# Optimization experiments

Measured on AMD Instinct MI355X. Metric: run time of the kernel, lower is better.

Reference implementation:

```python
import jax, jax.numpy as jnp
import numpy as np

N_NODES = 50000
N_EDGES = 1_600_000
FEAT, HIDDEN, NUM_CLASS = 128, 128, 64


def setup_inputs() -> dict:
    key = jax.random.key(0)
    k1, k2, k3, k4, k5 = jax.random.split(key, 5)
    h = jax.random.normal(k1, (N_NODES, FEAT), dtype=jnp.float32)
    edge_index = jax.random.randint(k2, (2, N_EDGES), 0, N_NODES, dtype=jnp.int32)
    # Glorot-ish init for the three GraphConv weights (bias=False)
    W1 = jax.random.normal(k3, (FEAT, HIDDEN), dtype=jnp.float32) * (1.0 / np.sqrt(FEAT))
    W2 = jax.random.normal(k4, (HIDDEN, HIDDEN), dtype=jnp.float32) * (1.0 / np.sqrt(HIDDEN))
    W3 = jax.random.normal(k5, (HIDDEN, NUM_CLASS), dtype=jnp.float32) * (1.0 / np.sqrt(HIDDEN))
    return {"h": h, "edge_index": edge_index, "W1": W1, "W2": W2, "W3": W3}


def _gcn_layer(h, W, src, dst, out_isqrt, in_isqrt, n_nodes):
    # DGL GraphConv, norm='both', bias=False: relu( D_in^{-1/2} A D_out^{-1/2} h W )
    h = h * out_isqrt[:, None]          # scale source features
    h = h @ W                            # dense projection (order-invariant)
    agg = jax.ops.segment_sum(h[src], dst, num_segments=n_nodes)  # SpMM aggregation
    agg = agg * in_isqrt[:, None]
    return jax.nn.relu(agg)


def reference(h, edge_index, W1, W2, W3):
    src, dst = edge_index[0], edge_index[1]
    ones = jnp.ones(src.shape[0], dtype=h.dtype)
    out_deg = jax.ops.segment_sum(ones, src, num_segments=N_NODES)
    in_deg = jax.ops.segment_sum(ones, dst, num_segments=N_NODES)
    out_isqrt = jnp.clip(out_deg, 1.0, None) ** -0.5
    in_isqrt = jnp.clip(in_deg, 1.0, None) ** -0.5
    h = _gcn_layer(h, W1, src, dst, out_isqrt, in_isqrt, N_NODES)
    h = _gcn_layer(h, W2, src, dst, out_isqrt, in_isqrt, N_NODES)
    h = _gcn_layer(h, W3, src, dst, out_isqrt, in_isqrt, N_NODES)
    return h
```

## Files before the change

### kernel.cpp

```cpp
#include <hip/hip_runtime.h>

#define N_NODES 50000
#define N_EDGES 1600000
#define FEAT 128
#define HIDDEN 128
#define NUM_CLASS 64

#define NBUCK 782
#define EPB 2048
#define NBLK 782
#define SCAP 2560
#define AGG_NBN 3125
#define GEMM_BLOCKS 782

#define HISTROW 50048
#define HISTW (HISTROW / 4)
#define HIST_EPB 6250

typedef _Float16 h8 __attribute__((ext_vector_type(8)));
typedef float f32x4 __attribute__((ext_vector_type(4)));

__global__ __launch_bounds__(256) void passA_kernel(const int* __restrict__ ei,
                                                    unsigned* __restrict__ priv,
                                                    int* __restrict__ localoff,
                                                    int* __restrict__ Cmat) {
    __shared__ int cnt[1024];
    __shared__ int base[1024];
    __shared__ int cur[1024];
    __shared__ int tmp[256];
    __shared__ unsigned sorted[EPB];
    const int t = threadIdx.x;
    const int blk = blockIdx.x;
    for (int i = t; i < 1024; i += 256) cnt[i] = 0;
    __syncthreads();

    const int ebase = blk * EPB;
    unsigned packed[8];
    int bk[8];
#pragma unroll
    for (int j = 0; j < 8; ++j) {
        const int e = ebase + t + j * 256;
        if (e < N_EDGES) {
            const unsigned s = (unsigned)ei[e];
            const unsigned d = (unsigned)ei[N_EDGES + e];
            bk[j] = (int)(d >> 6);
            packed[j] = s | ((d & 63u) << 16) | ((d >> 6) << 22);
            atomicAdd(&cnt[bk[j]], 1);
        } else bk[j] = -1;
    }
    __syncthreads();

    const int c0 = cnt[4*t], c1 = cnt[4*t+1], c2 = cnt[4*t+2], c3 = cnt[4*t+3];
    const int s = c0 + c1 + c2 + c3;
    tmp[t] = s;
    __syncthreads();
    for (int off = 1; off < 256; off <<= 1) {
        int v = (t >= off) ? tmp[t - off] : 0;
        __syncthreads();
        tmp[t] += v;
        __syncthreads();
    }
    const int excl = tmp[t] - s;
    base[4*t] = excl;            cur[4*t] = excl;
    base[4*t+1] = excl+c0;       cur[4*t+1] = excl+c0;
    base[4*t+2] = excl+c0+c1;    cur[4*t+2] = excl+c0+c1;
    base[4*t+3] = excl+c0+c1+c2; cur[4*t+3] = excl+c0+c1+c2;
    __syncthreads();

    for (int b = t; b < NBUCK; b += 256) {
        localoff[(size_t)blk * NBUCK + b] = base[b];
        Cmat[(size_t)blk * NBUCK + b] = cnt[b];
    }
#pragma unroll
    for (int j = 0; j < 8; ++j)
        if (bk[j] >= 0) {
            const int pos = atomicAdd(&cur[bk[j]], 1);
            sorted[pos] = packed[j];
        }
    __syncthreads();
    const int total = min(EPB, N_EDGES - ebase);
    for (int i = t; i < total; i += 256) priv[(size_t)blk * EPB + i] = sorted[i];
}

__global__ __launch_bounds__(256) void hist8_kernel(const int* __restrict__ ei,
                                                    unsigned* __restrict__ hist8) {
    __shared__ unsigned hh[HISTW];
    const int t = threadIdx.x;
    for (int i = t; i < HISTW; i += 256) hh[i] = 0;
    __syncthreads();
    const int base = blockIdx.x * HIST_EPB;
    for (int j = t; j < HIST_EPB; j += 256) {
        const unsigned s = (unsigned)ei[base + j];
        atomicAdd(&hh[s >> 2], 1u << ((s & 3u) * 8u));
    }
    __syncthreads();
    unsigned* dst = hist8 + (size_t)blockIdx.x * HISTW;
    for (int i = t; i < HISTW; i += 256) dst[i] = hh[i];
}

__global__ __launch_bounds__(256) void scales8_kernel(const unsigned* __restrict__ hist8,
                                                      float* __restrict__ out_isqrt) {
    const int w = blockIdx.x * 256 + threadIdx.x;
    if (w >= HISTW) return;
    unsigned s0 = 0, s1 = 0, s2 = 0, s3 = 0;
    for (int b = 0; b < 256; ++b) {
        const unsigned u = hist8[(size_t)b * HISTW + w];
        s0 += u & 255u; s1 += (u >> 8) & 255u; s2 += (u >> 16) & 255u; s3 += u >> 24;
    }
    const int n = w * 4;
    if (n < N_NODES)     out_isqrt[n]     = rsqrtf((float)(s0 < 1 ? 1 : s0));
    if (n + 1 < N_NODES) out_isqrt[n + 1] = rsqrtf((float)(s1 < 1 ? 1 : s1));
    if (n + 2 < N_NODES) out_isqrt[n + 2] = rsqrtf((float)(s2 < 1 ? 1 : s2));
    if (n + 3 < N_NODES) out_isqrt[n + 3] = rsqrtf((float)(s3 < 1 ? 1 : s3));
}

__global__ __launch_bounds__(256) void btotal_kernel(const int* __restrict__ Cmat,
                                                     int* __restrict__ total) {
    __shared__ int red[256];
    const int b = blockIdx.x;
    const int t = threadIdx.x;
    int s = 0;
    for (int blk = t; blk < NBLK; blk += 256) s += Cmat[(size_t)blk * NBUCK + b];
    red[t] = s;
    __syncthreads();
    for (int off = 128; off > 0; off >>= 1) {
        if (t < off) red[t] += red[t + off];
        __syncthreads();
    }
    if (t == 0) total[b] = red[0];
}

__global__ __launch_bounds__(256) void bscan2_kernel(const int* __restrict__ total,
                                                     int* __restrict__ csr_base,
                                                     int* __restrict__ row_off) {
    __shared__ int tt[1024];
    __shared__ int tmp[256];
    const int t = threadIdx.x;
    for (int i = t; i < 1024; i += 256) tt[i] = (i < NBUCK) ? total[i] : 0;
    __syncthreads();
    const int c0 = tt[4*t], c1 = tt[4*t+1], c2 = tt[4*t+2], c3 = tt[4*t+3];
    const int s = c0 + c1 + c2 + c3;
    tmp[t] = s;
    __syncthreads();
    for (int off = 1; off < 256; off <<= 1) {
        int v = (t >= off) ? tmp[t - off] : 0;
        __syncthreads();
        tmp[t] += v;
        __syncthreads();
    }
    const int excl = tmp[t] - s;
    if (4*t < NBUCK)   csr_base[4*t]   = excl;
    if (4*t+1 < NBUCK) csr_base[4*t+1] = excl + c0;
    if (4*t+2 < NBUCK) csr_base[4*t+2] = excl + c0 + c1;
    if (4*t+3 < NBUCK) csr_base[4*t+3] = excl + c0 + c1 + c2;
    if (t == 0) { csr_base[NBUCK] = N_EDGES; row_off[N_NODES] = N_EDGES; }
}

__global__ __launch_bounds__(256) void csr2_kernel(const int* __restrict__ localoff,
                                                   const unsigned* __restrict__ priv,
                                                   const int* __restrict__ csr_base,
                                                   unsigned short* __restrict__ csr,
                                                   int* __restrict__ row_off,
                                                   float* __restrict__ in_isqrt) {
    __shared__ unsigned gath[SCAP];
    __shared__ int tmp[256];
    __shared__ int cnt64[64];
    __shared__ int cur64[64];
    const int b = blockIdx.x;
    const int t = threadIdx.x;

    int off_[4], len_[4];
#pragma unroll
    for (int u = 0; u < 4; ++u) {
        const int blk = 4*t + u;
        if (blk < NBLK) {
            const int o = localoff[(size_t)blk * NBUCK + b];
            const int nxt = (b == NBUCK - 1) ? min(EPB, N_EDGES - blk * EPB)
                                             : localoff[(size_t)blk * NBUCK + b + 1];
            off_[u] = o; len_[u] = nxt - o;
        } else { off_[u] = 0; len_[u] = 0; }
    }
    const int s = len_[0] + len_[1] + len_[2] + len_[3];
    tmp[t] = s;
    __syncthreads();
    for (int off = 1; off < 256; off <<= 1) {
        int v = (t >= off) ? tmp[t - off] : 0;
        __syncthreads();
        tmp[t] += v;
        __syncthreads();
    }
    int run = tmp[t] - s;
    const int total = tmp[255];
#pragma unroll
    for (int u = 0; u < 4; ++u) {
        const int blk = 4*t + u;
        const unsigned* srcp = priv + (size_t)blk * EPB + off_[u];
        for (int j = 0; j < len_[u]; ++j)
            if (run + j < SCAP) gath[run + j] = srcp[j];
        run += len_[u];
    }
    if (t < 64) cnt64[t] = 0;
    __syncthreads();

    const int gtot = min(total, SCAP);
    for (int i = t; i < gtot; i += 256) atomicAdd(&cnt64[(gath[i] >> 16) & 63u], 1);
    __syncthreads();

    const int v64 = (t < 64) ? cnt64[t] : 0;
    tmp[t] = v64;
    __syncthreads();
    for (int off = 1; off < 64; off <<= 1) {
        int v = (t >= off) ? tmp[t - off] : 0;
        __syncthreads();
        tmp[t] += v;
        __syncthreads();
    }
    if (t < 64) {
        const int myoff = csr_base[b] + tmp[t] - v64;
        cur64[t] = myoff;
        const int node = b * 64 + t;
        if (node < N_NODES) {
            row_off[node] = myoff;
            in_isqrt[node] = rsqrtf((float)(v64 > 0 ? v64 : 1));
        }
    }
    __syncthreads();

    for (int i = t; i < gtot; i += 256) {
        const unsigned w = gath[i];
        const int pos = atomicAdd(&cur64[(w >> 16) & 63u], 1);
        csr[pos] = (unsigned short)(w & 0xFFFFu);
    }
}

__global__ __launch_bounds__(256) void wconv_kernel(const float* __restrict__ W1,
                                                    const float* __restrict__ W2,
                                                    const float* __restrict__ W3,
                                                    _Float16* __restrict__ WhT) {
    const int id = blockIdx.x * 256 + threadIdx.x;
    if (id < 16384) {
        const int n = id >> 7, k = id & 127;
        WhT[id] = (_Float16)W1[k * 128 + n];
    } else if (id < 32768) {
        const int i = id - 16384, n = i >> 7, k = i & 127;
        WhT[id] = (_Float16)W2[k * 128 + n];
    } else if (id < 40960) {
        const int i = id - 32768, n = i >> 7, k = i & 127;
        WhT[id] = (_Float16)W3[k * 64 + n];
    }
}

template <int OUT>
__global__ __launch_bounds__(256) void gemm_kernel(const float* __restrict__ H,
                                                   const _Float16* __restrict__ WhT,
                                                   const float* __restrict__ out_isqrt,
                                                   _Float16* __restrict__ Ys) {
    constexpr int NT = OUT / 16;
    __shared__ _Float16 Hs[64 * 128];
    char* hb = (char*)Hs;
    const int tid = threadIdx.x;
    const int bn = blockIdx.x * 64;

    {
        const int n = tid & 63, kg = tid >> 6;
        const int gn = bn + n;
        const int swz = (n & 7) << 4;
        if (gn < N_NODES) {
            const float4* hrow = (const float4*)(H + (size_t)gn * FEAT) + kg * 8;
#pragma unroll
            for (int jj = 0; jj < 4; ++jj) {
                const float4 u = hrow[jj * 2];
                const float4 v = hrow[jj * 2 + 1];
                h8 r;
                r[0] = (_Float16)u.x; r[1] = (_Float16)u.y; r[2] = (_Float16)u.z; r[3] = (_Float16)u.w;
                r[4] = (_Float16)v.x; r[5] = (_Float16)v.y; r[6] = (_Float16)v.z; r[7] = (_Float16)v.w;
                *(h8*)(hb + ((n * 256 + kg * 64 + jj * 16) ^ swz)) = r;
            }
        } else {
            h8 z;
#pragma unroll
            for (int i = 0; i < 8; ++i) z[i] = (_Float16)0.f;
#pragma unroll
            for (int jj = 0; jj < 4; ++jj)
                *(h8*)(hb + ((n * 256 + kg * 64 + jj * 16) ^ swz)) = z;
        }
    }
    __syncthreads();

    const int l = tid & 63, w = tid >> 6;
    const int lm = l & 15, lk = l >> 4;
    const int nloc = w * 16 + lm;
    const int swzr = (nloc & 7) << 4;

    h8 a[4];
#pragma unroll
    for (int kt = 0; kt < 4; ++kt)
        a[kt] = *(const h8*)(hb + ((nloc * 256 + (lk * 8 + kt * 32) * 2) ^ swzr));

    f32x4 acc[NT];
#pragma unroll
    for (int nt = 0; nt < NT; ++nt) acc[nt] = (f32x4){0.f, 0.f, 0.f, 0.f};

#pragma unroll
    for (int nt = 0; nt < NT; ++nt) {
        const _Float16* wp = WhT + (size_t)(nt * 16 + lm) * 128 + lk * 8;
#pragma unroll
        for (int kt = 0; kt < 4; ++kt) {
            const h8 b = *(const h8*)(wp + kt * 32);
            acc[nt] = __builtin_amdgcn_mfma_f32_16x16x32_f16(a[kt], b, acc[nt], 0, 0, 0);
        }
    }

#pragma unroll
    for (int r = 0; r < 4; ++r) {
        const int node = bn + w * 16 + lk * 4 + r;
        if (node < N_NODES) {
            const float sc = out_isqrt[node];
#pragma unroll
            for (int nt = 0; nt < NT; ++nt) {
                const int c = nt * 16 + lm;
                Ys[((size_t)(c >> 5) * N_NODES + node) * 32 + (c & 31)] = (_Float16)(acc[nt][r] * sc);
            }
        }
    }
}

template <int F>
__global__ __launch_bounds__(256) void agg_kernel(const int* __restrict__ row_off,
                                                  const unsigned short* __restrict__ csr,
                                                  const _Float16* __restrict__ Ys,
                                                  const float* __restrict__ in_isqrt,
                                                  float* __restrict__ out) {
    constexpr int NS = F / 32;
    const int s  = blockIdx.x & (NS - 1);
    const int nb = blockIdx.x / NS;
    const int tid = threadIdx.x;
    const int lane = tid & 63;
    const int j = lane >> 4;
    const int esub = (lane >> 2) & 3;
    const int q = lane & 3;

    const int d = nb * 16 + (tid >> 6) * 4 + j;
    const _Float16* Yp = Ys + (size_t)s * (N_NODES * 32) + q * 8;

    const int end = row_off[d + 1];
    float a0 = 0.f, a1 = 0.f, a2 = 0.f, a3 = 0.f, a4 = 0.f, a5 = 0.f, a6 = 0.f, a7 = 0.f;

    int e = row_off[d] + esub;
    for (; e + 4 < end; e += 8) {
        const int i0 = csr[e];
        const int i1 = csr[e + 4];
        const h8 v0 = *(const h8*)(Yp + (size_t)i0 * 32);
        const h8 v1 = *(const h8*)(Yp + (size_t)i1 * 32);
        a0 += (float)v0[0] + (float)v1[0];
        a1 += (float)v0[1] + (float)v1[1];
        a2 += (float)v0[2] + (float)v1[2];
        a3 += (float)v0[3] + (float)v1[3];
        a4 += (float)v0[4] + (float)v1[4];
        a5 += (float)v0[5] + (float)v1[5];
        a6 += (float)v0[6] + (float)v1[6];
        a7 += (float)v0[7] + (float)v1[7];
    }
    if (e < end) {
        const int i0 = csr[e];
        const h8 v0 = *(const h8*)(Yp + (size_t)i0 * 32);
        a0 += (float)v0[0]; a1 += (float)v0[1]; a2 += (float)v0[2]; a3 += (float)v0[3];
        a4 += (float)v0[4]; a5 += (float)v0[5]; a6 += (float)v0[6]; a7 += (float)v0[7];
    }

    a0 += __shfl_xor(a0, 4, 64); a0 += __shfl_xor(a0, 8, 64);
    a1 += __shfl_xor(a1, 4, 64); a1 += __shfl_xor(a1, 8, 64);
    a2 += __shfl_xor(a2, 4, 64); a2 += __shfl_xor(a2, 8, 64);
    a3 += __shfl_xor(a3, 4, 64); a3 += __shfl_xor(a3, 8, 64);
    a4 += __shfl_xor(a4, 4, 64); a4 += __shfl_xor(a4, 8, 64);
    a5 += __shfl_xor(a5, 4, 64); a5 += __shfl_xor(a5, 8, 64);
    a6 += __shfl_xor(a6, 4, 64); a6 += __shfl_xor(a6, 8, 64);
    a7 += __shfl_xor(a7, 4, 64); a7 += __shfl_xor(a7, 8, 64);

    if (esub == 0) {
        const float isq = in_isqrt[d];
        float4 r0, r1;
        r0.x = fmaxf(a0 * isq, 0.f); r0.y = fmaxf(a1 * isq, 0.f);
        r0.z = fmaxf(a2 * isq, 0.f); r0.w = fmaxf(a3 * isq, 0.f);
        r1.x = fmaxf(a4 * isq, 0.f); r1.y = fmaxf(a5 * isq, 0.f);
        r1.z = fmaxf(a6 * isq, 0.f); r1.w = fmaxf(a7 * isq, 0.f);
        float* op = out + (size_t)d * F + s * 32 + q * 8;
        *(float4*)op = r0;
        *(float4*)(op + 4) = r1;
    }
}

extern "C" void kernel_launch(void* const* d_in, const int* in_sizes, int n_in,
                              void* d_out, int out_size, void* d_ws, size_t ws_size,
                              hipStream_t stream) {
    const float* h  = (const float*)d_in[0];
    const int*   ei = (const int*)d_in[1];
    const float* W1 = (const float*)d_in[2];
    const float* W2 = (const float*)d_in[3];
    const float* W3 = (const float*)d_in[4];
    float* out = (float*)d_out;

    char* p = (char*)d_ws;
    auto alloc = [&p](size_t bytes) {
        void* r = (void*)p;
        p += (bytes + 255) & ~(size_t)255;
        return r;
    };
    int*   row_off  = (int*)alloc((N_NODES + 1) * sizeof(int));
    int*   csr_base = (int*)alloc((NBUCK + 1) * sizeof(int));
    int*   total    = (int*)alloc(NBUCK * sizeof(int));
    unsigned short* csr = (unsigned short*)alloc((size_t)N_EDGES * sizeof(unsigned short));
    float* in_isqrt  = (float*)alloc(N_NODES * sizeof(float));
    float* out_isqrt = (float*)alloc(N_NODES * sizeof(float));
    _Float16* WhT   = (_Float16*)alloc(40960 * sizeof(_Float16));
    _Float16* Ys    = (_Float16*)alloc((size_t)N_NODES * HIDDEN * sizeof(_Float16));
    float* bufA     = (float*)alloc((size_t)N_NODES * HIDDEN * sizeof(float));
    float* bufB     = (float*)alloc((size_t)N_NODES * HIDDEN * sizeof(float));
    unsigned* priv   = (unsigned*)bufA;
    int* localoff    = (int*)bufB;
    int* Cmat        = localoff + (size_t)NBLK * NBUCK;
    unsigned* hist8  = (unsigned*)((char*)bufB + (size_t)10 * 1024 * 1024);

    wconv_kernel<<<160, 256, 0, stream>>>(W1, W2, W3, WhT);
    passA_kernel<<<NBLK, 256, 0, stream>>>(ei, priv, localoff, Cmat);
    hist8_kernel<<<256, 256, 0, stream>>>(ei, hist8);
    btotal_kernel<<<NBUCK, 256, 0, stream>>>(Cmat, total);
    bscan2_kernel<<<1, 256, 0, stream>>>(total, csr_base, row_off);
    scales8_kernel<<<(HISTW + 255) / 256, 256, 0, stream>>>(hist8, out_isqrt);
    csr2_kernel<<<NBUCK, 256, 0, stream>>>(localoff, priv, csr_base, csr, row_off, in_isqrt);

    gemm_kernel<HIDDEN><<<GEMM_BLOCKS, 256, 0, stream>>>(h, WhT, out_isqrt, Ys);
    agg_kernel<HIDDEN><<<4 * AGG_NBN, 256, 0, stream>>>(row_off, csr, Ys, in_isqrt, bufA);

    gemm_kernel<HIDDEN><<<GEMM_BLOCKS, 256, 0, stream>>>(bufA, WhT + 16384, out_isqrt, Ys);
    agg_kernel<HIDDEN><<<4 * AGG_NBN, 256, 0, stream>>>(row_off, csr, Ys, in_isqrt, bufB);

    gemm_kernel<NUM_CLASS><<<GEMM_BLOCKS, 256, 0, stream>>>(bufB, WhT + 32768, out_isqrt, Ys);
    agg_kernel<NUM_CLASS><<<2 * AGG_NBN, 256, 0, stream>>>(row_off, csr, Ys, in_isqrt, out);
}
```

Before: 251.5 us.

## Store intermediate activations in fp16, swap MFMA operands, unroll aggregation, halve histogram shards

Intermediate layer outputs (bufA, bufB) are now stored as fp16 instead of fp32, which halves the write traffic in aggregation and the read traffic in the next GEMM, and lets the GEMM copy rows straight into shared memory without converting. The GEMM swaps its MFMA operands so each lane holds four consecutive features of one node and writes them as a single 4-wide fp16 store instead of scattered scalar stores. The aggregation loop gains a 4-way unrolled gather to keep more loads in flight. The degree histogram uses 128 shards instead of 256, and hist8 gets its own allocation. The fp16 intermediates add rounding error.

```diff
diff --git a/kernel.cpp b/kernel.cpp
--- a/kernel.cpp
+++ b/kernel.cpp
@@ -15,9 +15,11 @@
 
 #define HISTROW 50048
 #define HISTW (HISTROW / 4)
-#define HIST_EPB 6250
+#define NSHAD 128
+#define HIST_EPB 12500
 
 typedef _Float16 h8 __attribute__((ext_vector_type(8)));
+typedef _Float16 h4 __attribute__((ext_vector_type(4)));
 typedef float f32x4 __attribute__((ext_vector_type(4)));
 
 __global__ __launch_bounds__(256) void passA_kernel(const int* __restrict__ ei,
@@ -103,7 +105,7 @@
     const int w = blockIdx.x * 256 + threadIdx.x;
     if (w >= HISTW) return;
     unsigned s0 = 0, s1 = 0, s2 = 0, s3 = 0;
-    for (int b = 0; b < 256; ++b) {
+    for (int b = 0; b < NSHAD; ++b) {
         const unsigned u = hist8[(size_t)b * HISTW + w];
         s0 += u & 255u; s1 += (u >> 8) & 255u; s2 += (u >> 16) & 255u; s3 += u >> 24;
     }
@@ -250,8 +252,8 @@
     }
 }
 
-template <int OUT>
-__global__ __launch_bounds__(256) void gemm_kernel(const float* __restrict__ H,
+template <int OUT, typename InT>
+__global__ __launch_bounds__(256) void gemm_kernel(const InT* __restrict__ H,
                                                    const _Float16* __restrict__ WhT,
                                                    const float* __restrict__ out_isqrt,
                                                    _Float16* __restrict__ Ys) {
@@ -266,15 +268,22 @@
         const int gn = bn + n;
         const int swz = (n & 7) << 4;
         if (gn < N_NODES) {
-            const float4* hrow = (const float4*)(H + (size_t)gn * FEAT) + kg * 8;
-#pragma unroll
-            for (int jj = 0; jj < 4; ++jj) {
-                const float4 u = hrow[jj * 2];
-                const float4 v = hrow[jj * 2 + 1];
-                h8 r;
-                r[0] = (_Float16)u.x; r[1] = (_Float16)u.y; r[2] = (_Float16)u.z; r[3] = (_Float16)u.w;
-                r[4] = (_Float16)v.x; r[5] = (_Float16)v.y; r[6] = (_Float16)v.z; r[7] = (_Float16)v.w;
-                *(h8*)(hb + ((n * 256 + kg * 64 + jj * 16) ^ swz)) = r;
+            if constexpr (sizeof(InT) == 4) {
+                const float4* hrow = (const float4*)(H + (size_t)gn * FEAT) + kg * 8;
+#pragma unroll
+                for (int jj = 0; jj < 4; ++jj) {
+                    const float4 u = hrow[jj * 2];
+                    const float4 v = hrow[jj * 2 + 1];
+                    h8 r;
+                    r[0] = (_Float16)u.x; r[1] = (_Float16)u.y; r[2] = (_Float16)u.z; r[3] = (_Float16)u.w;
+                    r[4] = (_Float16)v.x; r[5] = (_Float16)v.y; r[6] = (_Float16)v.z; r[7] = (_Float16)v.w;
+                    *(h8*)(hb + ((n * 256 + kg * 64 + jj * 16) ^ swz)) = r;
+                }
+            } else {
+                const h8* hrow = (const h8*)(H + (size_t)gn * FEAT) + kg * 4;
+#pragma unroll
+                for (int jj = 0; jj < 4; ++jj)
+                    *(h8*)(hb + ((n * 256 + kg * 64 + jj * 16) ^ swz)) = hrow[jj];
             }
         } else {
             h8 z;
@@ -292,10 +301,10 @@
     const int nloc = w * 16 + lm;
     const int swzr = (nloc & 7) << 4;
 
-    h8 a[4];
+    h8 bfrag[4];
 #pragma unroll
     for (int kt = 0; kt < 4; ++kt)
-        a[kt] = *(const h8*)(hb + ((nloc * 256 + (lk * 8 + kt * 32) * 2) ^ swzr));
+        bfrag[kt] = *(const h8*)(hb + ((nloc * 256 + (lk * 8 + kt * 32) * 2) ^ swzr));
 
     f32x4 acc[NT];
 #pragma unroll
@@ -306,31 +315,33 @@
         const _Float16* wp = WhT + (size_t)(nt * 16 + lm) * 128 + lk * 8;
 #pragma unroll
         for (int kt = 0; kt < 4; ++kt) {
-            const h8 b = *(const h8*)(wp + kt * 32);
-            acc[nt] = __builtin_amdgcn_mfma_f32_16x16x32_f16(a[kt], b, acc[nt], 0, 0, 0);
-        }
-    }
-
-#pragma unroll
-    for (int r = 0; r < 4; ++r) {
-        const int node = bn + w * 16 + lk * 4 + r;
-        if (node < N_NODES) {
-            const float sc = out_isqrt[node];
-#pragma unroll
-            for (int nt = 0; nt < NT; ++nt) {
-                const int c = nt * 16 + lm;
-                Ys[((size_t)(c >> 5) * N_NODES + node) * 32 + (c & 31)] = (_Float16)(acc[nt][r] * sc);
-            }
-        }
-    }
-}
-
-template <int F>
+            const h8 afrag = *(const h8*)(wp + kt * 32);
+            acc[nt] = __builtin_amdgcn_mfma_f32_16x16x32_f16(afrag, bfrag[kt], acc[nt], 0, 0, 0);
+        }
+    }
+
+    const int node = bn + w * 16 + lm;
+    if (node < N_NODES) {
+        const float sc = out_isqrt[node];
+#pragma unroll
+        for (int nt = 0; nt < NT; ++nt) {
+            const int f0 = nt * 16 + lk * 4;
+            h4 r;
+            r[0] = (_Float16)(acc[nt][0] * sc);
+            r[1] = (_Float16)(acc[nt][1] * sc);
+            r[2] = (_Float16)(acc[nt][2] * sc);
+            r[3] = (_Float16)(acc[nt][3] * sc);
+            *(h4*)(Ys + ((size_t)(f0 >> 5) * N_NODES + node) * 32 + (f0 & 31)) = r;
+        }
+    }
+}
+
+template <int F, typename OT>
 __global__ __launch_bounds__(256) void agg_kernel(const int* __restrict__ row_off,
                                                   const unsigned short* __restrict__ csr,
                                                   const _Float16* __restrict__ Ys,
                                                   const float* __restrict__ in_isqrt,
-                                                  float* __restrict__ out) {
+                                                  OT* __restrict__ out) {
     constexpr int NS = F / 32;
     const int s  = blockIdx.x & (NS - 1);
     const int nb = blockIdx.x / NS;
@@ -347,6 +358,24 @@
     float a0 = 0.f, a1 = 0.f, a2 = 0.f, a3 = 0.f, a4 = 0.f, a5 = 0.f, a6 = 0.f, a7 = 0.f;
 
     int e = row_off[d] + esub;
+    for (; e + 12 < end; e += 16) {
+        const int i0 = csr[e];
+        const int i1 = csr[e + 4];
+        const int i2 = csr[e + 8];
+        const int i3 = csr[e + 12];
+        const h8 v0 = *(const h8*)(Yp + (size_t)i0 * 32);
+        const h8 v1 = *(const h8*)(Yp + (size_t)i1 * 32);
+        const h8 v2 = *(const h8*)(Yp + (size_t)i2 * 32);
+        const h8 v3 = *(const h8*)(Yp + (size_t)i3 * 32);
+        a0 += (float)v0[0] + (float)v1[0] + (float)v2[0] + (float)v3[0];
+        a1 += (float)v0[1] + (float)v1[1] + (float)v2[1] + (float)v3[1];
+        a2 += (float)v0[2] + (float)v1[2] + (float)v2[2] + (float)v3[2];
+        a3 += (float)v0[3] + (float)v1[3] + (float)v2[3] + (float)v3[3];
+        a4 += (float)v0[4] + (float)v1[4] + (float)v2[4] + (float)v3[4];
+        a5 += (float)v0[5] + (float)v1[5] + (float)v2[5] + (float)v3[5];
+        a6 += (float)v0[6] + (float)v1[6] + (float)v2[6] + (float)v3[6];
+        a7 += (float)v0[7] + (float)v1[7] + (float)v2[7] + (float)v3[7];
+    }
     for (; e + 4 < end; e += 8) {
         const int i0 = csr[e];
         const int i1 = csr[e + 4];
@@ -379,14 +408,21 @@
 
     if (esub == 0) {
         const float isq = in_isqrt[d];
-        float4 r0, r1;
-        r0.x = fmaxf(a0 * isq, 0.f); r0.y = fmaxf(a1 * isq, 0.f);
-        r0.z = fmaxf(a2 * isq, 0.f); r0.w = fmaxf(a3 * isq, 0.f);
-        r1.x = fmaxf(a4 * isq, 0.f); r1.y = fmaxf(a5 * isq, 0.f);
-        r1.z = fmaxf(a6 * isq, 0.f); r1.w = fmaxf(a7 * isq, 0.f);
-        float* op = out + (size_t)d * F + s * 32 + q * 8;
-        *(float4*)op = r0;
-        *(float4*)(op + 4) = r1;
+        const float r0 = fmaxf(a0 * isq, 0.f), r1 = fmaxf(a1 * isq, 0.f);
+        const float r2 = fmaxf(a2 * isq, 0.f), r3 = fmaxf(a3 * isq, 0.f);
+        const float r4 = fmaxf(a4 * isq, 0.f), r5 = fmaxf(a5 * isq, 0.f);
+        const float r6 = fmaxf(a6 * isq, 0.f), r7 = fmaxf(a7 * isq, 0.f);
+        if constexpr (sizeof(OT) == 2) {
+            h8 o;
+            o[0] = (_Float16)r0; o[1] = (_Float16)r1; o[2] = (_Float16)r2; o[3] = (_Float16)r3;
+            o[4] = (_Float16)r4; o[5] = (_Float16)r5; o[6] = (_Float16)r6; o[7] = (_Float16)r7;
+            *(h8*)((_Float16*)out + (size_t)d * F + s * 32 + q * 8) = o;
+        } else {
+            float* op = (float*)out + (size_t)d * F + s * 32 + q * 8;
+            float4 w0 = {r0, r1, r2, r3}, w1 = {r4, r5, r6, r7};
+            *(float4*)op = w0;
+            *(float4*)(op + 4) = w1;
+        }
     }
 }
 
@@ -414,27 +450,27 @@
     float* out_isqrt = (float*)alloc(N_NODES * sizeof(float));
     _Float16* WhT   = (_Float16*)alloc(40960 * sizeof(_Float16));
     _Float16* Ys    = (_Float16*)alloc((size_t)N_NODES * HIDDEN * sizeof(_Float16));
-    float* bufA     = (float*)alloc((size_t)N_NODES * HIDDEN * sizeof(float));
-    float* bufB     = (float*)alloc((size_t)N_NODES * HIDDEN * sizeof(float));
+    _Float16* bufA  = (_Float16*)alloc((size_t)N_NODES * HIDDEN * sizeof(_Float16));
+    _Float16* bufB  = (_Float16*)alloc((size_t)N_NODES * HIDDEN * sizeof(_Float16));
+    unsigned* hist8 = (unsigned*)alloc((size_t)NSHAD * HISTW * sizeof(unsigned));
     unsigned* priv   = (unsigned*)bufA;
     int* localoff    = (int*)bufB;
     int* Cmat        = localoff + (size_t)NBLK * NBUCK;
-    unsigned* hist8  = (unsigned*)((char*)bufB + (size_t)10 * 1024 * 1024);
 
     wconv_kernel<<<160, 256, 0, stream>>>(W1, W2, W3, WhT);
     passA_kernel<<<NBLK, 256, 0, stream>>>(ei, priv, localoff, Cmat);
-    hist8_kernel<<<256, 256, 0, stream>>>(ei, hist8);
+    hist8_kernel<<<NSHAD, 256, 0, stream>>>(ei, hist8);
     btotal_kernel<<<NBUCK, 256, 0, stream>>>(Cmat, total);
     bscan2_kernel<<<1, 256, 0, stream>>>(total, csr_base, row_off);
     scales8_kernel<<<(HISTW + 255) / 256, 256, 0, stream>>>(hist8, out_isqrt);
     csr2_kernel<<<NBUCK, 256, 0, stream>>>(localoff, priv, csr_base, csr, row_off, in_isqrt);
 
-    gemm_kernel<HIDDEN><<<GEMM_BLOCKS, 256, 0, stream>>>(h, WhT, out_isqrt, Ys);
-    agg_kernel<HIDDEN><<<4 * AGG_NBN, 256, 0, stream>>>(row_off, csr, Ys, in_isqrt, bufA);
-
-    gemm_kernel<HIDDEN><<<GEMM_BLOCKS, 256, 0, stream>>>(bufA, WhT + 16384, out_isqrt, Ys);
-    agg_kernel<HIDDEN><<<4 * AGG_NBN, 256, 0, stream>>>(row_off, csr, Ys, in_isqrt, bufB);
-
-    gemm_kernel<NUM_CLASS><<<GEMM_BLOCKS, 256, 0, stream>>>(bufB, WhT + 32768, out_isqrt, Ys);
-    agg_kernel<NUM_CLASS><<<2 * AGG_NBN, 256, 0, stream>>>(row_off, csr, Ys, in_isqrt, out);
-}
+    gemm_kernel<HIDDEN, float><<<GEMM_BLOCKS, 256, 0, stream>>>(h, WhT, out_isqrt, Ys);
+    agg_kernel<HIDDEN, _Float16><<<4 * AGG_NBN, 256, 0, stream>>>(row_off, csr, Ys, in_isqrt, bufA);
+
+    gemm_kernel<HIDDEN, _Float16><<<GEMM_BLOCKS, 256, 0, stream>>>(bufA, WhT + 16384, out_isqrt, Ys);
+    agg_kernel<HIDDEN, _Float16><<<4 * AGG_NBN, 256, 0, stream>>>(row_off, csr, Ys, in_isqrt, bufB);
+
+    gemm_kernel<NUM_CLASS, _Float16><<<GEMM_BLOCKS, 256, 0, stream>>>(bufB, WhT + 32768, out_isqrt, Ys);
+    agg_kernel<NUM_CLASS, float><<<2 * AGG_NBN, 256, 0, stream>>>(row_off, csr, Ys, in_isqrt, out);
+}
```

Result: faster. 241.0 us (-4.2%).
